# Kernel optimization log

Measured on AMD Instinct MI355X. Metric: run time of the kernel, lower is better.

## Reference

```python
import jax, jax.numpy as jnp
import numpy as np

EMBED_DIM = 1024
BATCH = 4
SEQ = 2048


def setup_inputs() -> dict:
    key = jax.random.key(0)
    ks = jax.random.split(key, 9)
    D = EMBED_DIM
    s = 1.0 / np.sqrt(D)
    inputs = jax.random.normal(ks[0], (BATCH, SEQ, D), dtype=jnp.float32)
    rotation_params = jax.random.normal(ks[1], (D, D), dtype=jnp.float32) * s
    entangle_params = jax.random.normal(ks[2], (D, D), dtype=jnp.float32) * s
    Wq = jax.random.normal(ks[3], (D, D), dtype=jnp.float32) * s
    bq = jax.random.normal(ks[4], (D,), dtype=jnp.float32) * 0.01
    Wk = jax.random.normal(ks[5], (D, D), dtype=jnp.float32) * s
    bk = jax.random.normal(ks[6], (D,), dtype=jnp.float32) * 0.01
    Wv = jax.random.normal(ks[7], (D, D), dtype=jnp.float32) * s
    bv = jax.random.normal(ks[8], (D,), dtype=jnp.float32) * 0.01
    # causal mask: True = masked out (matches torch masked_fill semantics)
    mask = jnp.triu(jnp.ones((SEQ, SEQ), dtype=bool), k=1)
    return {"inputs": inputs, "rotation_params": rotation_params,
            "entangle_params": entangle_params, "Wq": Wq, "bq": bq,
            "Wk": Wk, "bk": bk, "Wv": Wv, "bv": bv, "mask": mask}


def reference(inputs, rotation_params, entangle_params, Wq, bq, Wk, bk, Wv, bv, mask):
    D = inputs.shape[-1]
    # q = Linear(x) @ R^T ; k = Linear(x) @ E^T ; v = Linear(x)
    q = (jnp.einsum('bsd,ed->bse', inputs, Wq) + bq) @ rotation_params.T
    k = (jnp.einsum('bsd,ed->bse', inputs, Wk) + bk) @ entangle_params.T
    v = jnp.einsum('bsd,ed->bse', inputs, Wv) + bv
    scores = jnp.einsum('bqd,bkd->bqk', q, k) / jnp.sqrt(jnp.float32(D))
    scores = jnp.where(mask, jnp.float32(-jnp.inf), scores)
    probs = jax.nn.softmax(scores, axis=-1)  # dropout=0.0 -> identity
    return jnp.einsum('bqk,bkd->bqd', probs, v)
```

## Files before the change

kernel.cpp:

```cpp
#include <hip/hip_runtime.h>
#include <hip/hip_bf16.h>
#include <stdint.h>

#define DD 1024
#define SS 2048
#define BB 4

typedef __bf16 bf16;
typedef __bf16 bf16x8 __attribute__((ext_vector_type(8)));
typedef __bf16 bf16x4 __attribute__((ext_vector_type(4)));
typedef float f32x4 __attribute__((ext_vector_type(4)));

__device__ __forceinline__ void gload_lds16(const bf16* g, bf16* l) {
  __builtin_amdgcn_global_load_lds(
      (const __attribute__((address_space(1))) void*)g,
      (__attribute__((address_space(3))) void*)l, 16, 0, 0);
}

__global__ void cvt_f32_bf16(const float* __restrict__ src,
                             bf16* __restrict__ dst, int n) {
  int i = (blockIdx.x * blockDim.x + threadIdx.x) * 4;
  if (i >= n) return;
  float4 v = *(const float4*)(src + i);
  bf16x4 o;
  o.x = (bf16)v.x; o.y = (bf16)v.y; o.z = (bf16)v.z; o.w = (bf16)v.w;
  *(bf16x4*)(dst + i) = o;
}

__global__ void transpose_cvt(const float* __restrict__ src,
                              bf16* __restrict__ dst) {
  __shared__ float tile[32][33];
  int x = blockIdx.x * 32 + threadIdx.x;
  int y0 = blockIdx.y * 32;
  for (int r = threadIdx.y; r < 32; r += 8)
    tile[r][threadIdx.x] = src[(y0 + r) * DD + x];
  __syncthreads();
  int dx = blockIdx.y * 32 + threadIdx.x;
  int dy0 = blockIdx.x * 32;
  for (int r = threadIdx.y; r < 32; r += 8)
    dst[(dy0 + r) * DD + dx] = (bf16)tile[threadIdx.x][r];
}

__global__ void transpose_v(const bf16* __restrict__ qkv,
                            bf16* __restrict__ vT) {
  __shared__ bf16 tile[32][33];
  int b = blockIdx.z;
  int d0 = blockIdx.x * 32, s0 = blockIdx.y * 32;
  const bf16* src = qkv + (long)b * SS * 3072 + 2048;
  for (int r = threadIdx.y; r < 32; r += 8)
    tile[r][threadIdx.x] = src[(long)(s0 + r) * 3072 + d0 + threadIdx.x];
  __syncthreads();
  bf16* dst = vT + (long)b * DD * SS;
  for (int r = threadIdx.y; r < 32; r += 8)
    dst[(long)(d0 + r) * SS + s0 + threadIdx.x] = tile[threadIdx.x][r];
}

__global__ void bias_fold(const float* __restrict__ R, const float* __restrict__ bq,
                          const float* __restrict__ E, const float* __restrict__ bk,
                          const float* __restrict__ bv, float* __restrict__ bias) {
  int e = blockIdx.x;
  if (e >= 2048) { if (threadIdx.x == 0) bias[e] = bv[e - 2048]; return; }
  const float* M = (e < 1024) ? R : E;
  const float* bb = (e < 1024) ? bq : bk;
  int row = e & 1023;
  float s = 0.f;
  for (int f = threadIdx.x; f < DD; f += 256) s += M[row * DD + f] * bb[f];
  for (int o = 32; o >= 1; o >>= 1) s += __shfl_xor(s, o, 64);
  __shared__ float red[4];
  if ((threadIdx.x & 63) == 0) red[threadIdx.x >> 6] = s;
  __syncthreads();
  if (threadIdx.x == 0) bias[e] = red[0] + red[1] + red[2] + red[3];
}

template <int MODE>
__global__ __launch_bounds__(256, 4)
void gemm_bt(const bf16* __restrict__ Ag, long lda, long sAb,
             const bf16* __restrict__ Bg, long ldb, long sBb,
             void* __restrict__ Cg, long ldc, long sCb,
             const float* __restrict__ bias, float scale, int K) {
  __shared__ __align__(16) bf16 As[128 * 32];
  __shared__ __align__(16) bf16 Bs[128 * 32];

  int bx = blockIdx.x, by = blockIdx.y, bz = blockIdx.z;
  if (MODE == 1 && bx > by) return;
  long m0 = (long)by * 128, n0 = (long)bx * 128;
  const bf16* A = Ag + (long)bz * sAb + m0 * lda;
  const bf16* Bp = Bg + (long)bz * sBb + n0 * ldb;

  int t = threadIdx.x;
  int w = t >> 6, l = t & 63;
  int lr = l >> 2;
  int lc = (((l & 3) ^ (lr & 3)) * 8);
  int quad = l >> 4, ln = l & 15;
  int wm = w >> 1, wn = w & 1;
  int rdoff = ((quad ^ (ln & 3)) * 8);

  int Keff = (MODE == 2) ? (by + 1) * 128 : K;

  f32x4 acc[4][4];
#pragma unroll
  for (int i = 0; i < 4; i++)
#pragma unroll
    for (int j = 0; j < 4; j++) acc[i][j] = f32x4{0.f, 0.f, 0.f, 0.f};

  const bf16* a_base = As + (wm * 64 + ln) * 32 + rdoff;
  const bf16* b_base = Bs + (wn * 64 + ln) * 32 + rdoff;
  long arow0 = (long)(w * 16 + lr);

  for (int k0 = 0; k0 < Keff; k0 += 32) {
    gload_lds16(A + arow0 * lda + k0 + lc, As + w * 512);
    gload_lds16(A + (arow0 + 64) * lda + k0 + lc, As + 2048 + w * 512);
    gload_lds16(Bp + arow0 * ldb + k0 + lc, Bs + w * 512);
    gload_lds16(Bp + (arow0 + 64) * ldb + k0 + lc, Bs + 2048 + w * 512);
    asm volatile("s_waitcnt vmcnt(0)" ::: "memory");
    __syncthreads();

    bf16x8 af[4], bfr[4];
#pragma unroll
    for (int i = 0; i < 4; i++) {
      af[i] = *(const bf16x8*)(a_base + i * 512);
      bfr[i] = *(const bf16x8*)(b_base + i * 512);
    }
#pragma unroll
    for (int i = 0; i < 4; i++)
#pragma unroll
      for (int j = 0; j < 4; j++)
        acc[i][j] = __builtin_amdgcn_mfma_f32_16x16x32_bf16(af[i], bfr[j],
                                                            acc[i][j], 0, 0, 0);
    __syncthreads();
  }

  if (MODE == 0) {
    bf16* C = (bf16*)Cg + (long)bz * sCb + m0 * ldc + n0;
#pragma unroll
    for (int i = 0; i < 4; i++) {
      int rb = wm * 64 + i * 16 + quad * 4;
#pragma unroll
      for (int j = 0; j < 4; j++) {
        int col = wn * 64 + j * 16 + ln;
        float bv_ = bias ? bias[n0 + col] : 0.f;
#pragma unroll
        for (int r = 0; r < 4; r++)
          C[(long)(rb + r) * ldc + col] = (bf16)(acc[i][j][r] + bv_);
      }
    }
  } else {
    float* C = (float*)Cg + (long)bz * sCb + m0 * ldc + n0;
#pragma unroll
    for (int i = 0; i < 4; i++) {
      int rb = wm * 64 + i * 16 + quad * 4;
#pragma unroll
      for (int j = 0; j < 4; j++) {
        int col = wn * 64 + j * 16 + ln;
#pragma unroll
        for (int r = 0; r < 4; r++) {
          int row = rb + r;
          if (MODE == 1) {
            if (n0 + col <= m0 + row)
              C[(long)row * ldc + col] = acc[i][j][r] * scale;
          } else {
            C[(long)row * ldc + col] = acc[i][j][r];
          }
        }
      }
    }
  }
}

__global__ __launch_bounds__(256) void softmax_rows(float* __restrict__ scores) {
  long m = blockIdx.x;
  int i = (int)(m & (SS - 1));
  float* row = scores + m * SS;
  int t = threadIdx.x;
  int nvalid = i + 1;
  int base = t * 8;
  float x[8] = {0, 0, 0, 0, 0, 0, 0, 0};
  if (base < nvalid) {
    float4 v0 = *(const float4*)(row + base);
    float4 v1 = *(const float4*)(row + base + 4);
    x[0] = v0.x; x[1] = v0.y; x[2] = v0.z; x[3] = v0.w;
    x[4] = v1.x; x[5] = v1.y; x[6] = v1.z; x[7] = v1.w;
  }

  float mx = -INFINITY;
#pragma unroll
  for (int j = 0; j < 8; j++)
    if (base + j < nvalid) mx = fmaxf(mx, x[j]);
  for (int o = 32; o >= 1; o >>= 1) mx = fmaxf(mx, __shfl_xor(mx, o, 64));
  __shared__ float red[8];
  if ((t & 63) == 0) red[t >> 6] = mx;
  __syncthreads();
  mx = fmaxf(fmaxf(red[0], red[1]), fmaxf(red[2], red[3]));

  float e[8];
  float sum = 0.f;
#pragma unroll
  for (int j = 0; j < 8; j++) {
    e[j] = (base + j < nvalid) ? __expf(x[j] - mx) : 0.f;
    sum += e[j];
  }
  for (int o = 32; o >= 1; o >>= 1) sum += __shfl_xor(sum, o, 64);
  if ((t & 63) == 0) red[4 + (t >> 6)] = sum;
  __syncthreads();
  sum = red[4] + red[5] + red[6] + red[7];
  float inv = 1.f / sum;

  bf16x8 o8;
#pragma unroll
  for (int j = 0; j < 8; j++) o8[j] = (bf16)(e[j] * inv);
  *(bf16x8*)((bf16*)row + base) = o8;
}

extern "C" void kernel_launch(void* const* d_in, const int* in_sizes, int n_in,
                              void* d_out, int out_size, void* d_ws,
                              size_t ws_size, hipStream_t stream) {
  const float* x = (const float*)d_in[0];
  const float* R = (const float*)d_in[1];
  const float* E = (const float*)d_in[2];
  const float* Wq = (const float*)d_in[3];
  const float* bq = (const float*)d_in[4];
  const float* Wk = (const float*)d_in[5];
  const float* bk = (const float*)d_in[6];
  const float* Wv = (const float*)d_in[7];
  const float* bv = (const float*)d_in[8];
  float* out = (float*)d_out;

  char* ws = (char*)d_ws;
  bf16* qkv = (bf16*)ws;
  bf16* vT = (bf16*)(ws + 50331648);
  float* scores = (float*)(ws + 67108864);
  char* sr = ws + 67108864;
  bf16* xb = (bf16*)sr;
  bf16* Rb = (bf16*)(sr + 16777216);
  bf16* WqT = (bf16*)(sr + 20971520);
  bf16* wcat = (bf16*)(sr + 25165824);
  float* bias = (float*)(sr + 31457280);
  bf16* Eb = Rb + 1024 * 1024;
  bf16* WkT = WqT + 1024 * 1024;

  cvt_f32_bf16<<<8192, 256, 0, stream>>>(x, xb, BB * SS * DD);
  cvt_f32_bf16<<<1024, 256, 0, stream>>>(R, Rb, DD * DD);
  cvt_f32_bf16<<<1024, 256, 0, stream>>>(E, Eb, DD * DD);
  cvt_f32_bf16<<<1024, 256, 0, stream>>>(Wv, wcat + 2048 * DD, DD * DD);
  transpose_cvt<<<dim3(32, 32), dim3(32, 8), 0, stream>>>(Wq, WqT);
  transpose_cvt<<<dim3(32, 32), dim3(32, 8), 0, stream>>>(Wk, WkT);
  bias_fold<<<3072, 256, 0, stream>>>(R, bq, E, bk, bv, bias);

  gemm_bt<0><<<dim3(8, 8, 2), 256, 0, stream>>>(
      Rb, DD, 1024 * 1024, WqT, DD, 1024 * 1024, wcat, DD, 1024 * 1024,
      nullptr, 1.f, DD);

  gemm_bt<0><<<dim3(24, 64, 1), 256, 0, stream>>>(xb, DD, 0, wcat, DD, 0, qkv,
                                                  3072, 0, bias, 1.f, DD);

  transpose_v<<<dim3(32, 64, BB), dim3(32, 8), 0, stream>>>(qkv, vT);

  gemm_bt<1><<<dim3(16, 16, BB), 256, 0, stream>>>(
      qkv, 3072, (long)SS * 3072, qkv + 1024, 3072, (long)SS * 3072, scores,
      SS, (long)SS * SS, nullptr, 0.03125f, DD);

  softmax_rows<<<BB * SS, 256, 0, stream>>>(scores);

  gemm_bt<2><<<dim3(8, 16, BB), 256, 0, stream>>>(
      (const bf16*)scores, 4096, (long)SS * 4096, vT, SS, (long)DD * SS, out,
      DD, (long)SS * DD, nullptr, 1.f, SS);
}
```

Measured before the change: 350.0 us.

## Merge conversion launches, fuse V transpose into QKV GEMM, deepen K tile

Combines the four f32-to-bf16 conversion launches into one kernel and the two weight transposes into a single launch. Removes the separate V transpose pass by having the QKV GEMM write the V block transposed through shared memory. Doubles the per-iteration K depth of the GEMM to 64, halving barriers per K step while doubling LDS use to 32KB per block, which may reduce occupancy.

Measured after the change: 311.5 us. 11.0% less time.

```diff
diff --git a/kernel.cpp b/kernel.cpp
--- a/kernel.cpp
+++ b/kernel.cpp
@@ -17,18 +17,30 @@
       (__attribute__((address_space(3))) void*)l, 16, 0, 0);
 }
 
-__global__ void cvt_f32_bf16(const float* __restrict__ src,
-                             bf16* __restrict__ dst, int n) {
-  int i = (blockIdx.x * blockDim.x + threadIdx.x) * 4;
-  if (i >= n) return;
+__global__ void cvt_all(const float* __restrict__ x, const float* __restrict__ R,
+                        const float* __restrict__ E, const float* __restrict__ Wv,
+                        bf16* __restrict__ xb, bf16* __restrict__ Rb,
+                        bf16* __restrict__ Eb, bf16* __restrict__ Wvb) {
+  int bid = blockIdx.x;
+  const float* src;
+  bf16* dst;
+  int base;
+  if (bid < 8192) { src = x; dst = xb; base = bid; }
+  else if (bid < 9216) { src = R; dst = Rb; base = bid - 8192; }
+  else if (bid < 10240) { src = E; dst = Eb; base = bid - 9216; }
+  else { src = Wv; dst = Wvb; base = bid - 10240; }
+  int i = (base * 256 + threadIdx.x) * 4;
   float4 v = *(const float4*)(src + i);
   bf16x4 o;
   o.x = (bf16)v.x; o.y = (bf16)v.y; o.z = (bf16)v.z; o.w = (bf16)v.w;
   *(bf16x4*)(dst + i) = o;
 }
 
-__global__ void transpose_cvt(const float* __restrict__ src,
-                              bf16* __restrict__ dst) {
+__global__ void transpose_cvt(const float* __restrict__ Wq,
+                              const float* __restrict__ Wk,
+                              bf16* __restrict__ WqT, bf16* __restrict__ WkT) {
+  const float* src = blockIdx.z ? Wk : Wq;
+  bf16* dst = blockIdx.z ? WkT : WqT;
   __shared__ float tile[32][33];
   int x = blockIdx.x * 32 + threadIdx.x;
   int y0 = blockIdx.y * 32;
@@ -39,20 +51,6 @@
   int dy0 = blockIdx.x * 32;
   for (int r = threadIdx.y; r < 32; r += 8)
     dst[(dy0 + r) * DD + dx] = (bf16)tile[threadIdx.x][r];
-}
-
-__global__ void transpose_v(const bf16* __restrict__ qkv,
-                            bf16* __restrict__ vT) {
-  __shared__ bf16 tile[32][33];
-  int b = blockIdx.z;
-  int d0 = blockIdx.x * 32, s0 = blockIdx.y * 32;
-  const bf16* src = qkv + (long)b * SS * 3072 + 2048;
-  for (int r = threadIdx.y; r < 32; r += 8)
-    tile[r][threadIdx.x] = src[(long)(s0 + r) * 3072 + d0 + threadIdx.x];
-  __syncthreads();
-  bf16* dst = vT + (long)b * DD * SS;
-  for (int r = threadIdx.y; r < 32; r += 8)
-    dst[(long)(d0 + r) * SS + s0 + threadIdx.x] = tile[threadIdx.x][r];
 }
 
 __global__ void bias_fold(const float* __restrict__ R, const float* __restrict__ bq,
@@ -77,9 +75,11 @@
 void gemm_bt(const bf16* __restrict__ Ag, long lda, long sAb,
              const bf16* __restrict__ Bg, long ldb, long sBb,
              void* __restrict__ Cg, long ldc, long sCb,
-             const float* __restrict__ bias, float scale, int K) {
-  __shared__ __align__(16) bf16 As[128 * 32];
-  __shared__ __align__(16) bf16 Bs[128 * 32];
+             const float* __restrict__ bias, float scale, int K,
+             bf16* __restrict__ vTp) {
+  __shared__ __align__(16) bf16 smem[16384];
+  bf16* As = smem;
+  bf16* Bs = smem + 8192;
 
   int bx = blockIdx.x, by = blockIdx.y, bz = blockIdx.z;
   if (MODE == 1 && bx > by) return;
@@ -107,41 +107,75 @@
   const bf16* b_base = Bs + (wn * 64 + ln) * 32 + rdoff;
   long arow0 = (long)(w * 16 + lr);
 
-  for (int k0 = 0; k0 < Keff; k0 += 32) {
-    gload_lds16(A + arow0 * lda + k0 + lc, As + w * 512);
-    gload_lds16(A + (arow0 + 64) * lda + k0 + lc, As + 2048 + w * 512);
-    gload_lds16(Bp + arow0 * ldb + k0 + lc, Bs + w * 512);
-    gload_lds16(Bp + (arow0 + 64) * ldb + k0 + lc, Bs + 2048 + w * 512);
+  for (int k0 = 0; k0 < Keff; k0 += 64) {
+#pragma unroll
+    for (int kk = 0; kk < 2; kk++) {
+      int kc = k0 + kk * 32 + lc;
+      gload_lds16(A + arow0 * lda + kc, As + kk * 4096 + w * 512);
+      gload_lds16(A + (arow0 + 64) * lda + kc, As + kk * 4096 + 2048 + w * 512);
+      gload_lds16(Bp + arow0 * ldb + kc, Bs + kk * 4096 + w * 512);
+      gload_lds16(Bp + (arow0 + 64) * ldb + kc, Bs + kk * 4096 + 2048 + w * 512);
+    }
     asm volatile("s_waitcnt vmcnt(0)" ::: "memory");
     __syncthreads();
 
-    bf16x8 af[4], bfr[4];
-#pragma unroll
-    for (int i = 0; i < 4; i++) {
-      af[i] = *(const bf16x8*)(a_base + i * 512);
-      bfr[i] = *(const bf16x8*)(b_base + i * 512);
-    }
-#pragma unroll
-    for (int i = 0; i < 4; i++)
-#pragma unroll
-      for (int j = 0; j < 4; j++)
-        acc[i][j] = __builtin_amdgcn_mfma_f32_16x16x32_bf16(af[i], bfr[j],
-                                                            acc[i][j], 0, 0, 0);
+#pragma unroll
+    for (int kk = 0; kk < 2; kk++) {
+      bf16x8 af[4], bfr[4];
+#pragma unroll
+      for (int i = 0; i < 4; i++) {
+        af[i] = *(const bf16x8*)(a_base + kk * 4096 + i * 512);
+        bfr[i] = *(const bf16x8*)(b_base + kk * 4096 + i * 512);
+      }
+#pragma unroll
+      for (int i = 0; i < 4; i++)
+#pragma unroll
+        for (int j = 0; j < 4; j++)
+          acc[i][j] = __builtin_amdgcn_mfma_f32_16x16x32_bf16(
+              af[i], bfr[j], acc[i][j], 0, 0, 0);
+    }
     __syncthreads();
   }
 
   if (MODE == 0) {
-    bf16* C = (bf16*)Cg + (long)bz * sCb + m0 * ldc + n0;
-#pragma unroll
-    for (int i = 0; i < 4; i++) {
-      int rb = wm * 64 + i * 16 + quad * 4;
-#pragma unroll
-      for (int j = 0; j < 4; j++) {
-        int col = wn * 64 + j * 16 + ln;
-        float bv_ = bias ? bias[n0 + col] : 0.f;
-#pragma unroll
-        for (int r = 0; r < 4; r++)
-          C[(long)(rb + r) * ldc + col] = (bf16)(acc[i][j][r] + bv_);
+    if (vTp && n0 >= 2048) {
+      int d0 = (int)n0 - 2048;
+      int b = (int)(m0 >> 11);
+      int s0 = (int)(m0 & 2047);
+#pragma unroll
+      for (int i = 0; i < 4; i++) {
+        int sb = wm * 64 + i * 16 + quad * 4;
+#pragma unroll
+        for (int j = 0; j < 4; j++) {
+          int d = wn * 64 + j * 16 + ln;
+          float bv_ = bias[n0 + d];
+#pragma unroll
+          for (int r = 0; r < 4; r++)
+            smem[d * 128 + ((sb + r) ^ (ln << 3))] = (bf16)(acc[i][j][r] + bv_);
+        }
+      }
+      __syncthreads();
+      int d = t >> 1, h = t & 1;
+      bf16* dst = vTp + (long)b * DD * SS + (long)(d0 + d) * SS + s0 + h * 64;
+#pragma unroll
+      for (int j = 0; j < 8; j++) {
+        int sbase = h * 64 + j * 8;
+        bf16x8 v = *(const bf16x8*)(smem + d * 128 + (sbase ^ ((d & 15) << 3)));
+        *(bf16x8*)(dst + j * 8) = v;
+      }
+    } else {
+      bf16* C = (bf16*)Cg + (long)bz * sCb + m0 * ldc + n0;
+#pragma unroll
+      for (int i = 0; i < 4; i++) {
+        int rb = wm * 64 + i * 16 + quad * 4;
+#pragma unroll
+        for (int j = 0; j < 4; j++) {
+          int col = wn * 64 + j * 16 + ln;
+          float bv_ = bias ? bias[n0 + col] : 0.f;
+#pragma unroll
+          for (int r = 0; r < 4; r++)
+            C[(long)(rb + r) * ldc + col] = (bf16)(acc[i][j][r] + bv_);
+        }
       }
     }
   } else {
@@ -238,30 +272,24 @@
   bf16* Eb = Rb + 1024 * 1024;
   bf16* WkT = WqT + 1024 * 1024;
 
-  cvt_f32_bf16<<<8192, 256, 0, stream>>>(x, xb, BB * SS * DD);
-  cvt_f32_bf16<<<1024, 256, 0, stream>>>(R, Rb, DD * DD);
-  cvt_f32_bf16<<<1024, 256, 0, stream>>>(E, Eb, DD * DD);
-  cvt_f32_bf16<<<1024, 256, 0, stream>>>(Wv, wcat + 2048 * DD, DD * DD);
-  transpose_cvt<<<dim3(32, 32), dim3(32, 8), 0, stream>>>(Wq, WqT);
-  transpose_cvt<<<dim3(32, 32), dim3(32, 8), 0, stream>>>(Wk, WkT);
+  cvt_all<<<11264, 256, 0, stream>>>(x, R, E, Wv, xb, Rb, Eb, wcat + 2048 * DD);
+  transpose_cvt<<<dim3(32, 32, 2), dim3(32, 8), 0, stream>>>(Wq, Wk, WqT, WkT);
   bias_fold<<<3072, 256, 0, stream>>>(R, bq, E, bk, bv, bias);
 
   gemm_bt<0><<<dim3(8, 8, 2), 256, 0, stream>>>(
       Rb, DD, 1024 * 1024, WqT, DD, 1024 * 1024, wcat, DD, 1024 * 1024,
-      nullptr, 1.f, DD);
+      nullptr, 1.f, DD, nullptr);
 
   gemm_bt<0><<<dim3(24, 64, 1), 256, 0, stream>>>(xb, DD, 0, wcat, DD, 0, qkv,
-                                                  3072, 0, bias, 1.f, DD);
-
-  transpose_v<<<dim3(32, 64, BB), dim3(32, 8), 0, stream>>>(qkv, vT);
+                                                  3072, 0, bias, 1.f, DD, vT);
 
   gemm_bt<1><<<dim3(16, 16, BB), 256, 0, stream>>>(
       qkv, 3072, (long)SS * 3072, qkv + 1024, 3072, (long)SS * 3072, scores,
-      SS, (long)SS * SS, nullptr, 0.03125f, DD);
+      SS, (long)SS * SS, nullptr, 0.03125f, DD, nullptr);
 
   softmax_rows<<<BB * SS, 256, 0, stream>>>(scores);
 
   gemm_bt<2><<<dim3(8, 16, BB), 256, 0, stream>>>(
       (const bf16*)scores, 4096, (long)SS * 4096, vT, SS, (long)DD * SS, out,
-      DD, (long)SS * DD, nullptr, 1.f, SS);
-}
+      DD, (long)SS * DD, nullptr, 1.f, SS, nullptr);
+}
```
